# Performance work log

Measured on AMD Instinct MI355X. Metric: run time of the kernel, lower is better.

Reference implementation:

```python
import jax, jax.numpy as jnp
import numpy as np

D_MODEL = 1024
NHEAD = 16
D_K = D_MODEL // NHEAD
EPS = 1e-5


def _layernorm(x, scale, bias):
    m = jnp.mean(x, axis=-1, keepdims=True)
    v = jnp.var(x, axis=-1, keepdims=True)
    return (x - m) * jax.lax.rsqrt(v + EPS) * scale + bias


def setup_inputs() -> dict:
    key = jax.random.key(0)
    ks = jax.random.split(key, 16)
    d, h = D_MODEL, 4 * D_MODEL
    s = 1.0 / np.sqrt(d)
    inp = {
        "x": jax.random.normal(ks[0], (2, 2048, d), dtype=jnp.float32),
        "Wq": jax.random.normal(ks[1], (d, d), dtype=jnp.float32) * s,
        "bq": jnp.zeros((d,), jnp.float32),
        "Wk": jax.random.normal(ks[2], (d, d), dtype=jnp.float32) * s,
        "bk": jnp.zeros((d,), jnp.float32),
        "Wv": jax.random.normal(ks[3], (d, d), dtype=jnp.float32) * s,
        "bv": jnp.zeros((d,), jnp.float32),
        "Wo": jax.random.normal(ks[4], (d, d), dtype=jnp.float32) * s,
        "bo": jnp.zeros((d,), jnp.float32),
        "ln1_scale": jnp.ones((d,), jnp.float32),
        "ln1_bias": jnp.zeros((d,), jnp.float32),
        "ln2_scale": jnp.ones((d,), jnp.float32),
        "ln2_bias": jnp.zeros((d,), jnp.float32),
        "W1": jax.random.normal(ks[5], (d, h), dtype=jnp.float32) * s,
        "b1": jnp.zeros((h,), jnp.float32),
        "W2": jax.random.normal(ks[6], (h, d), dtype=jnp.float32) * (1.0 / np.sqrt(h)),
        "b2": jnp.zeros((d,), jnp.float32),
    }
    return inp


def reference(x, Wq, bq, Wk, bk, Wv, bv, Wo, bo,
              ln1_scale, ln1_bias, ln2_scale, ln2_bias,
              W1, b1, W2, b2):
    batch, seq, d_model = x.shape
    # Faithful to original: q is viewed WITHOUT transpose (asymmetric vs k,v)
    q = (x @ Wq + bq).reshape(batch, NHEAD, seq, D_K)
    k = (x @ Wk + bk).reshape(batch, seq, NHEAD, D_K).transpose(0, 2, 1, 3)
    v = (x @ Wv + bv).reshape(batch, seq, NHEAD, D_K).transpose(0, 2, 1, 3)
    # scores: [B, H, S, S]
    scores = jnp.einsum('bhqd,bhkd->bhqk', q, k) / np.sqrt(D_K)
    attn = jax.nn.softmax(scores, axis=-1)
    o = jnp.einsum('bhqk,bhkd->bhqd', attn, v)  # [B,H,S,dk]
    o = o.transpose(0, 2, 1, 3).reshape(batch, seq, d_model)
    x = _layernorm(x + o @ Wo + bo, ln1_scale, ln1_bias)
    ff = jax.nn.relu(x @ W1 + b1) @ W2 + b2
    x = _layernorm(x + ff, ln2_scale, ln2_bias)
    return x
```

## Files before the change

kernel.cpp:

```cpp
#include <hip/hip_runtime.h>
#include <cstdint>

typedef __bf16 bf16x8 __attribute__((ext_vector_type(8)));
typedef float  floatx4 __attribute__((ext_vector_type(4)));

__device__ __forceinline__ unsigned short f2bf(float x) {
  union { float f; uint32_t u; } v; v.f = x;
  uint32_t r = (v.u + 0x7FFFu + ((v.u >> 16) & 1u)) >> 16;
  return (unsigned short)r;
}
__device__ __forceinline__ float bflo(uint32_t u) {
  union { uint32_t u; float f; } v; v.u = u << 16; return v.f;
}
__device__ __forceinline__ float bfhi(uint32_t u) {
  union { uint32_t u; float f; } v; v.u = u & 0xffff0000u; return v.f;
}
__device__ __forceinline__ float bfu(unsigned short u) {
  union { uint32_t u; float f; } v; v.u = (uint32_t)u << 16; return v.f;
}

__device__ __forceinline__ void async_copy16(const void* g, void* l) {
  __builtin_amdgcn_global_load_lds(
      (const __attribute__((address_space(1))) uint32_t*)g,
      (__attribute__((address_space(3))) uint32_t*)l, 16, 0, 0);
}

template<int OUT_BF16, int RELU>
__global__ __launch_bounds__(256, 2)
void gemm_bt_kernel(const unsigned short* __restrict__ A,
                    const unsigned short* __restrict__ Bt,
                    void* __restrict__ C, const float* __restrict__ bias,
                    int M, int N, int K, int Kper) {
  __shared__ __align__(16) unsigned short l0A[128 * 32];
  __shared__ __align__(16) unsigned short l0B[128 * 32];
  __shared__ __align__(16) unsigned short l1A[128 * 32];
  __shared__ __align__(16) unsigned short l1B[128 * 32];
  const int tid  = threadIdx.x;
  const int wave = tid >> 6;
  const int lane = tid & 63;

  const int gx = gridDim.x, gy = gridDim.y;
  int flat = blockIdx.y * gx + blockIdx.x;
  const int per = (gx * gy) >> 3;
  flat = (flat & 7) * per + (flat >> 3);
  const int sq = flat >> 6, inner = flat & 63;
  const int sqm = gy >> 3;
  const int m0 = ((sq % sqm) * 8 + (inner & 7)) * 128;
  const int n0 = ((sq / sqm) * 8 + (inner >> 3)) * 128;

  const int kz = blockIdx.z;
  const int wm = (wave >> 1) * 64;
  const int wn = (wave & 1) * 64;
  const int sa_row = lane >> 2;
  const int sa_k   = ((lane & 3) ^ ((lane >> 3) & 3)) * 8;
  const int fr = lane & 15;
  const int fq = lane >> 4;
  const int sw = (fr >> 1) & 3;

  const int r0 = (wave * 2 + 0) * 16 + sa_row;
  const int r1 = (wave * 2 + 1) * 16 + sa_row;
  const unsigned short* A0 = A  + (size_t)(m0 + r0) * K + kz * Kper + sa_k;
  const unsigned short* A1 = A  + (size_t)(m0 + r1) * K + kz * Kper + sa_k;
  const unsigned short* B0 = Bt + (size_t)(n0 + r0) * K + kz * Kper + sa_k;
  const unsigned short* B1 = Bt + (size_t)(n0 + r1) * K + kz * Kper + sa_k;

  floatx4 acc[4][4];
  #pragma unroll
  for (int i = 0; i < 4; ++i)
    #pragma unroll
    for (int j = 0; j < 4; ++j)
      acc[i][j] = (floatx4){0.f, 0.f, 0.f, 0.f};

  const int c0 = (wave * 2 + 0) * 512;
  const int c1 = (wave * 2 + 1) * 512;

#define PREFETCH(kt, LA, LB)                                   \
  do {                                                         \
    const int koff = (kt) << 5;                                \
    async_copy16(A0 + koff, &(LA)[c0]);                        \
    async_copy16(A1 + koff, &(LA)[c1]);                        \
    async_copy16(B0 + koff, &(LB)[c0]);                        \
    async_copy16(B1 + koff, &(LB)[c1]);                        \
  } while (0)

#define COMPUTE(LA, LB)                                                        \
  do {                                                                         \
    bf16x8 af[4], bf[4];                                                       \
    _Pragma("unroll")                                                          \
    for (int t = 0; t < 4; ++t) {                                              \
      af[t] = *(const bf16x8*)&(LA)[(wm + t * 16 + fr) * 32 + (fq ^ sw) * 8];  \
      bf[t] = *(const bf16x8*)&(LB)[(wn + t * 16 + fr) * 32 + (fq ^ sw) * 8];  \
    }                                                                          \
    _Pragma("unroll")                                                          \
    for (int mt = 0; mt < 4; ++mt)                                             \
      _Pragma("unroll")                                                        \
      for (int nt = 0; nt < 4; ++nt)                                           \
        acc[mt][nt] = __builtin_amdgcn_mfma_f32_16x16x32_bf16(af[mt], bf[nt],  \
                                                              acc[mt][nt], 0, 0, 0); \
  } while (0)

  const int kIters = Kper >> 5;
  PREFETCH(0, l0A, l0B);
  for (int kt = 0; kt < kIters; kt += 2) {
    PREFETCH(kt + 1, l1A, l1B);
    asm volatile("s_waitcnt vmcnt(4)" ::: "memory");
    asm volatile("s_barrier" ::: "memory");
    COMPUTE(l0A, l0B);
    asm volatile("s_barrier" ::: "memory");
    if (kt + 2 < kIters) {
      PREFETCH(kt + 2, l0A, l0B);
      asm volatile("s_waitcnt vmcnt(4)" ::: "memory");
    } else {
      asm volatile("s_waitcnt vmcnt(0)" ::: "memory");
    }
    asm volatile("s_barrier" ::: "memory");
    COMPUTE(l1A, l1B);
    asm volatile("s_barrier" ::: "memory");
  }
#undef PREFETCH
#undef COMPUTE

  const float* bp = (kz == 0) ? bias : nullptr;
  char* Cz = (char*)C + (size_t)kz * M * N * (OUT_BF16 ? 2 : 4);
  #pragma unroll
  for (int mt = 0; mt < 4; ++mt) {
    #pragma unroll
    for (int nt = 0; nt < 4; ++nt) {
      const int gn = n0 + wn + nt * 16 + fr;
      const float bv = bp ? bp[gn] : 0.f;
      #pragma unroll
      for (int r = 0; r < 4; ++r) {
        const int gm = m0 + wm + mt * 16 + fq * 4 + r;
        float v = acc[mt][nt][r] + bv;
        if (RELU) v = fmaxf(v, 0.f);
        if (OUT_BF16) ((unsigned short*)Cz)[(size_t)gm * N + gn] = f2bf(v);
        else          ((float*)Cz)[(size_t)gm * N + gn] = v;
      }
    }
  }
}

__global__ __launch_bounds__(256, 2)
void gemm_oproj_kernel(const unsigned short* __restrict__ Opart,
                       const float* __restrict__ invL,
                       const unsigned short* __restrict__ Bt,
                       unsigned short* __restrict__ C,
                       const float* __restrict__ bias) {
  const int K = 1024, N = 1024, M = 4096, Kper = 512;
  __shared__ __align__(16) unsigned short lA[128 * 32];
  __shared__ __align__(16) unsigned short lB[128 * 32];
  const int tid  = threadIdx.x;
  const int wave = tid >> 6;
  const int lane = tid & 63;

  const int gx = gridDim.x, gy = gridDim.y;
  int flat = blockIdx.y * gx + blockIdx.x;
  const int per = (gx * gy) >> 3;
  flat = (flat & 7) * per + (flat >> 3);
  const int sq = flat >> 6, inner = flat & 63;
  const int sqm = gy >> 3;
  const int m0 = ((sq % sqm) * 8 + (inner & 7)) * 128;
  const int n0 = ((sq / sqm) * 8 + (inner >> 3)) * 128;

  const int kz = blockIdx.z;
  const int wm = (wave >> 1) * 64;
  const int wn = (wave & 1) * 64;
  const int sa_row = lane >> 2;
  const int sa_k   = ((lane & 3) ^ ((lane >> 3) & 3)) * 8;
  const int fr = lane & 15;
  const int fq = lane >> 4;
  const int sw = (fr >> 1) & 3;

  const int r0 = (wave * 2 + 0) * 16 + sa_row;
  const int r1 = (wave * 2 + 1) * 16 + sa_row;
  const int gm0 = m0 + r0, gm1 = m0 + r1;
  const int base0 = (gm0 >> 11) * 16 * 2048 + (gm0 & 2047);
  const int base1 = (gm1 >> 11) * 16 * 2048 + (gm1 & 2047);
  const unsigned short* B0 = Bt + (size_t)(n0 + r0) * K + kz * Kper + sa_k;
  const unsigned short* B1 = Bt + (size_t)(n0 + r1) * K + kz * Kper + sa_k;
  const int c0 = (wave * 2 + 0) * 512;
  const int c1 = (wave * 2 + 1) * 512;

  floatx4 acc[4][4];
  #pragma unroll
  for (int i = 0; i < 4; ++i)
    #pragma unroll
    for (int j = 0; j < 4; ++j)
      acc[i][j] = (floatx4){0.f, 0.f, 0.f, 0.f};

  for (int kt = 0; kt < 16; ++kt) {
    __syncthreads();
    const int kk = kz * Kper + (kt << 5) + sa_k;
    const int h = kk >> 6, d0 = kk & 63;
    #pragma unroll
    for (int j = 0; j < 2; ++j) {
      const int base = j ? base1 : base0;
      const int cj   = j ? c1 : c0;
      const int rowi = base + h * 2048;
      const size_t idx = (size_t)rowi * 64 + d0;
      const uint4 a = *(const uint4*)(Opart + idx);
      const uint4 b = *(const uint4*)(Opart + idx + 4194304);
      const float s = invL[rowi];
      const uint32_t au[4] = {a.x, a.y, a.z, a.w};
      const uint32_t bu[4] = {b.x, b.y, b.z, b.w};
      uint32_t w[4];
      #pragma unroll
      for (int k = 0; k < 4; ++k) {
        const float lo = (bflo(au[k]) + bflo(bu[k])) * s;
        const float hi = (bfhi(au[k]) + bfhi(bu[k])) * s;
        w[k] = (uint32_t)f2bf(lo) | ((uint32_t)f2bf(hi) << 16);
      }
      uint4 wv; wv.x = w[0]; wv.y = w[1]; wv.z = w[2]; wv.w = w[3];
      *(uint4*)&lA[cj + lane * 8] = wv;
    }
    async_copy16(B0 + (kt << 5), &lB[c0]);
    async_copy16(B1 + (kt << 5), &lB[c1]);
    __syncthreads();

    bf16x8 af[4], bf[4];
    #pragma unroll
    for (int t = 0; t < 4; ++t) {
      af[t] = *(const bf16x8*)&lA[(wm + t * 16 + fr) * 32 + (fq ^ sw) * 8];
      bf[t] = *(const bf16x8*)&lB[(wn + t * 16 + fr) * 32 + (fq ^ sw) * 8];
    }
    #pragma unroll
    for (int mt = 0; mt < 4; ++mt)
      #pragma unroll
      for (int nt = 0; nt < 4; ++nt)
        acc[mt][nt] = __builtin_amdgcn_mfma_f32_16x16x32_bf16(af[mt], bf[nt], acc[mt][nt], 0, 0, 0);
  }

  const float* bp = (kz == 0) ? bias : nullptr;
  unsigned short* Cz = C + (size_t)kz * M * N;
  #pragma unroll
  for (int mt = 0; mt < 4; ++mt) {
    #pragma unroll
    for (int nt = 0; nt < 4; ++nt) {
      const int gn = n0 + wn + nt * 16 + fr;
      const float bv = bp ? bp[gn] : 0.f;
      #pragma unroll
      for (int r = 0; r < 4; ++r) {
        const int gm = m0 + wm + mt * 16 + fq * 4 + r;
        Cz[(size_t)gm * N + gn] = f2bf(acc[mt][nt][r] + bv);
      }
    }
  }
}

__global__ __launch_bounds__(256)
void repack_v_kernel(const unsigned short* __restrict__ X,
                     unsigned short* __restrict__ Vt) {
  const int bid = blockIdx.x;
  const int st = bid & 31, h = (bid >> 5) & 15, b = bid >> 9;
  const int bh = b * 16 + h;
  const int s0 = st * 64;
  const int t = threadIdx.x;
  const int sl = t >> 2;
  const int c  = (t & 3) * 16;
  __shared__ __align__(16) unsigned short vt[64][72];
  {
    const uint4* srcV = (const uint4*)(X + (size_t)(b * 2048 + s0 + sl) * 3072 + 2048 + h * 64 + c);
    uint4* dstL = (uint4*)&vt[sl][c];
    dstL[0] = srcV[0]; dstL[1] = srcV[1];
  }
  __syncthreads();
  const int d = t >> 2, cc = (t & 3) * 16;
  unsigned short tmp[16];
  #pragma unroll
  for (int j = 0; j < 16; ++j) {
    const int chat = cc + j;
    const int key = (chat & 3) * 16 + (chat >> 2);
    tmp[j] = vt[key][d];
  }
  uint4* dstV = (uint4*)(Vt + ((size_t)bh * 64 + d) * 2048 + s0 + cc);
  dstV[0] = *(uint4*)&tmp[0];
  dstV[1] = *(uint4*)&tmp[8];
}

__global__ __launch_bounds__(256, 4)
void flash_attn_kernel(const unsigned short* __restrict__ QKVb,
                       const unsigned short* __restrict__ Vt,
                       unsigned short* __restrict__ Opart, float* __restrict__ Lpart) {
  const int bid = blockIdx.x;
  const int qt = bid & 15, h = (bid >> 4) & 15, b = (bid >> 8) & 1, ksp = bid >> 9;
  const int bh = b * 16 + h;
  const int wave = threadIdx.x >> 6, lane = threadIdx.x & 63;
  const int fr = lane & 15, fq = lane >> 4;

  __shared__ __align__(16) unsigned short lK[64 * 64];
  __shared__ __align__(16) unsigned short lV[64 * 64];
  __shared__ __align__(16) unsigned short lP[4][32 * 72];

  const int q_base = qt * 128 + wave * 32;
  bf16x8 aq[2][2];
  #pragma unroll
  for (int g = 0; g < 2; ++g) {
    const int s2 = q_base + g * 16 + fr;
    const unsigned short* qp = QKVb + (size_t)(b * 2048 + h * 128 + (s2 >> 4)) * 3072
                             + (s2 & 15) * 64 + fq * 8;
    aq[g][0] = *(const bf16x8*)qp;
    aq[g][1] = *(const bf16x8*)(qp + 32);
  }
  floatx4 o_acc[2][4];
  #pragma unroll
  for (int g = 0; g < 2; ++g)
    #pragma unroll
    for (int nt = 0; nt < 4; ++nt) o_acc[g][nt] = (floatx4){0.f, 0.f, 0.f, 0.f};
  float lrow[2][4];
  #pragma unroll
  for (int g = 0; g < 2; ++g)
    #pragma unroll
    for (int r = 0; r < 4; ++r) lrow[g][r] = 0.f;

  const unsigned short* Kg = QKVb + 1024 + h * 64;
  const unsigned short* Vg = Vt + (size_t)bh * 64 * 2048;

  const int srow = lane >> 3;
  const int scol = ((lane & 7) ^ (lane >> 3)) * 8;
  const int sw = fr & 7;
  const int ch0 = wave * 2, ch1 = wave * 2 + 1;
  const int krow0 = ch0 * 8 + srow, krow1 = ch1 * 8 + srow;

  for (int kt = ksp * 16; kt < ksp * 16 + 16; ++kt) {
    __syncthreads();
    async_copy16(Kg + (size_t)(b * 2048 + kt * 64 + krow0) * 3072 + scol, (char*)lK + ch0 * 1024);
    async_copy16(Vg + (size_t)krow0 * 2048 + kt * 64 + scol,              (char*)lV + ch0 * 1024);
    async_copy16(Kg + (size_t)(b * 2048 + kt * 64 + krow1) * 3072 + scol, (char*)lK + ch1 * 1024);
    async_copy16(Vg + (size_t)krow1 * 2048 + kt * 64 + scol,              (char*)lV + ch1 * 1024);
    asm volatile("s_waitcnt vmcnt(0)" ::: "memory");
    __syncthreads();

    floatx4 s_acc[2][4];
    #pragma unroll
    for (int nt = 0; nt < 4; ++nt) {
      const int row = (nt * 16 + fr) * 64;
      bf16x8 bk0 = *(const bf16x8*)&lK[row + ((0 + fq) ^ sw) * 8];
      bf16x8 bk1 = *(const bf16x8*)&lK[row + ((4 + fq) ^ sw) * 8];
      #pragma unroll
      for (int g = 0; g < 2; ++g) {
        floatx4 acc = (floatx4){0.f, 0.f, 0.f, 0.f};
        acc = __builtin_amdgcn_mfma_f32_16x16x32_bf16(aq[g][0], bk0, acc, 0, 0, 0);
        acc = __builtin_amdgcn_mfma_f32_16x16x32_bf16(aq[g][1], bk1, acc, 0, 0, 0);
        s_acc[g][nt] = acc;
      }
    }
    bf16x8 bvv[2][4];
    #pragma unroll
    for (int kk = 0; kk < 2; ++kk)
      #pragma unroll
      for (int nt = 0; nt < 4; ++nt)
        bvv[kk][nt] = *(const bf16x8*)&lV[(nt * 16 + fr) * 64 + ((kk * 4 + fq) ^ sw) * 8];

    #pragma unroll
    for (int g = 0; g < 2; ++g) {
      #pragma unroll
      for (int r = 0; r < 4; ++r) {
        const float p0 = __builtin_amdgcn_exp2f(s_acc[g][0][r] * 0.18033688f);
        const float p1 = __builtin_amdgcn_exp2f(s_acc[g][1][r] * 0.18033688f);
        const float p2 = __builtin_amdgcn_exp2f(s_acc[g][2][r] * 0.18033688f);
        const float p3 = __builtin_amdgcn_exp2f(s_acc[g][3][r] * 0.18033688f);
        lrow[g][r] += (p0 + p1) + (p2 + p3);
        union { float f; uint32_t u; } c0, c1, c2, c3;
        c0.f = p0; c1.f = p1; c2.f = p2; c3.f = p3;
        uint2 pk;
        pk.x = (c1.u & 0xffff0000u) | (c0.u >> 16);
        pk.y = (c3.u & 0xffff0000u) | (c2.u >> 16);
        *(uint2*)&lP[wave][(g * 16 + fq * 4 + r) * 72 + fr * 4] = pk;
      }
    }
    #pragma unroll
    for (int g = 0; g < 2; ++g) {
      #pragma unroll
      for (int kk = 0; kk < 2; ++kk) {
        bf16x8 ap = *(const bf16x8*)&lP[wave][(g * 16 + fr) * 72 + kk * 32 + fq * 8];
        #pragma unroll
        for (int nt = 0; nt < 4; ++nt)
          o_acc[g][nt] = __builtin_amdgcn_mfma_f32_16x16x32_bf16(ap, bvv[kk][nt], o_acc[g][nt], 0, 0, 0);
      }
    }
  }

  const size_t rbase = (size_t)ksp * 65536 + (size_t)bh * 2048 + q_base;
  #pragma unroll
  for (int g = 0; g < 2; ++g) {
    #pragma unroll
    for (int r = 0; r < 4; ++r) {
      float l = lrow[g][r];
      #pragma unroll
      for (int off = 1; off < 16; off <<= 1) l += __shfl_xor(l, off);
      if (fr == 0) Lpart[rbase + g * 16 + fq * 4 + r] = l;
    }
    #pragma unroll
    for (int nt = 0; nt < 4; ++nt)
      #pragma unroll
      for (int r = 0; r < 4; ++r)
        Opart[(rbase + g * 16 + fq * 4 + r) * 64 + nt * 16 + fr] = f2bf(o_acc[g][nt][r]);
  }
}

__global__ __launch_bounds__(256)
void invl_kernel(const float* __restrict__ Lpart, float* __restrict__ invL) {
  const int i = blockIdx.x * 256 + threadIdx.x;
  invL[i] = 1.f / (Lpart[i] + Lpart[i + 65536]);
}

template<int XF32, int OUTF32>
__global__ __launch_bounds__(256)
void ln_kernel(const void* __restrict__ Xv, const unsigned short* __restrict__ R,
               const unsigned short* __restrict__ R2,
               const float* __restrict__ sc, const float* __restrict__ bi,
               float* __restrict__ outF, unsigned short* __restrict__ outB) {
  const int row = blockIdx.x;
  const int t = threadIdx.x;
  const size_t base = (size_t)row * 1024 + t * 4;
  float4 a;
  if (XF32) {
    a = *(const float4*)((const float*)Xv + base);
  } else {
    const ushort4 xu = *(const ushort4*)((const unsigned short*)Xv + base);
    a.x = bfu(xu.x); a.y = bfu(xu.y); a.z = bfu(xu.z); a.w = bfu(xu.w);
  }
  const ushort4 r1u = *(const ushort4*)&R[base];
  const ushort4 r2u = *(const ushort4*)&R2[base];
  a.x += bfu(r1u.x) + bfu(r2u.x);
  a.y += bfu(r1u.y) + bfu(r2u.y);
  a.z += bfu(r1u.z) + bfu(r2u.z);
  a.w += bfu(r1u.w) + bfu(r2u.w);
  float sum = (a.x + a.y) + (a.z + a.w);
  float sq  = (a.x * a.x + a.y * a.y) + (a.z * a.z + a.w * a.w);
  #pragma unroll
  for (int off = 32; off > 0; off >>= 1) {
    sum += __shfl_down(sum, off);
    sq  += __shfl_down(sq, off);
  }
  __shared__ float s1[4], s2a[4];
  const int wave = t >> 6, lane = t & 63;
  if (lane == 0) { s1[wave] = sum; s2a[wave] = sq; }
  __syncthreads();
  sum = (s1[0] + s1[1]) + (s1[2] + s1[3]);
  sq  = (s2a[0] + s2a[1]) + (s2a[2] + s2a[3]);
  const float mean = sum * (1.f / 1024.f);
  const float var  = sq * (1.f / 1024.f) - mean * mean;
  const float rstd = rsqrtf(var + 1e-5f);
  const float4 s = *(const float4*)&sc[t * 4];
  const float4 bb = *(const float4*)&bi[t * 4];
  float4 y;
  y.x = (a.x - mean) * rstd * s.x + bb.x;
  y.y = (a.y - mean) * rstd * s.y + bb.y;
  y.z = (a.z - mean) * rstd * s.z + bb.z;
  y.w = (a.w - mean) * rstd * s.w + bb.w;
  if (OUTF32) {
    *(float4*)&outF[base] = y;
  } else {
    ushort4 ob; ob.x = f2bf(y.x); ob.y = f2bf(y.y); ob.z = f2bf(y.z); ob.w = f2bf(y.w);
    *(ushort4*)&outB[base] = ob;
  }
}

__global__ void prep_kernel(const float* __restrict__ Wq, const float* __restrict__ Wk,
                            const float* __restrict__ Wv, const float* __restrict__ Wo,
                            const float* __restrict__ W1, const float* __restrict__ W2,
                            unsigned short* __restrict__ Wqkvt, unsigned short* __restrict__ Wot,
                            unsigned short* __restrict__ W1t, unsigned short* __restrict__ W2t,
                            const float* __restrict__ x, unsigned short* __restrict__ xb,
                            const float* __restrict__ bq, const float* __restrict__ bk,
                            const float* __restrict__ bv, float* __restrict__ bqkv) {
  const int id = blockIdx.x;
  const int tflat = threadIdx.y * 32 + threadIdx.x;
  if (id >= 16384) {
    const int i = (id - 16384) * 256 + tflat;
    if (i < 1024) bqkv[i] = bq[i];
    else if (i < 2048) bqkv[i] = bk[i - 1024];
    else if (i < 3072) bqkv[i] = bv[i - 2048];
    return;
  }
  if (id >= 12288) {
    const int i = (id - 12288) * 256 + tflat;
    const float4 v = ((const float4*)x)[i];
    ushort4 o;
    o.x = f2bf(v.x); o.y = f2bf(v.y); o.z = f2bf(v.z); o.w = f2bf(v.w);
    ((ushort4*)xb)[i] = o;
    return;
  }
  const float* W; unsigned short* Wt; int K, N, tile;
  if (id < 4096) {
    const int w = id >> 10; tile = id & 1023; K = 1024; N = 1024;
    if (w == 0)      { W = Wq; Wt = Wqkvt; }
    else if (w == 1) { W = Wk; Wt = Wqkvt + 1024 * 1024; }
    else if (w == 2) { W = Wv; Wt = Wqkvt + 2048 * 1024; }
    else             { W = Wo; Wt = Wot; }
  } else if (id < 8192) { tile = id - 4096; W = W1; Wt = W1t; K = 1024; N = 4096; }
  else                  { tile = id - 8192; W = W2; Wt = W2t; K = 4096; N = 1024; }
  const int tilesX = N >> 5;
  const int bx = (tile & (tilesX - 1)) * 32;
  const int by = (tile / tilesX) * 32;
  __shared__ float tl[32][33];
  const int tx = threadIdx.x, ty = threadIdx.y;
  #pragma unroll
  for (int i = ty; i < 32; i += 8)
    tl[i][tx] = W[(size_t)(by + i) * N + bx + tx];
  __syncthreads();
  #pragma unroll
  for (int i = ty; i < 32; i += 8)
    Wt[(size_t)(bx + i) * K + by + tx] = f2bf(tl[tx][i]);
}

extern "C" void kernel_launch(void* const* d_in, const int* in_sizes, int n_in,
                              void* d_out, int out_size, void* d_ws, size_t ws_size,
                              hipStream_t stream) {
  const float* x    = (const float*)d_in[0];
  const float* Wq   = (const float*)d_in[1];
  const float* bq   = (const float*)d_in[2];
  const float* Wk   = (const float*)d_in[3];
  const float* bk   = (const float*)d_in[4];
  const float* Wv   = (const float*)d_in[5];
  const float* bv   = (const float*)d_in[6];
  const float* Wo   = (const float*)d_in[7];
  const float* bo   = (const float*)d_in[8];
  const float* ln1s = (const float*)d_in[9];
  const float* ln1b = (const float*)d_in[10];
  const float* ln2s = (const float*)d_in[11];
  const float* ln2b = (const float*)d_in[12];
  const float* W1   = (const float*)d_in[13];
  const float* b1   = (const float*)d_in[14];
  const float* W2   = (const float*)d_in[15];
  const float* b2   = (const float*)d_in[16];
  float* out = (float*)d_out;

  char* ws = (char*)d_ws;
  const size_t MB = 1u << 20;
  unsigned short* QKVb = (unsigned short*)(ws + 0);
  unsigned short* t1   = (unsigned short*)(ws + 0);
  unsigned short* ffh  = (unsigned short*)(ws + 0);
  unsigned short* Vt   = (unsigned short*)(ws + 32 * MB);
  unsigned short* ff   = (unsigned short*)(ws + 32 * MB);
  unsigned short* xb   = (unsigned short*)(ws + 48 * MB);
  unsigned short* Opart= (unsigned short*)(ws + 48 * MB);
  unsigned short* Wqkvt= (unsigned short*)(ws + 56 * MB);
  float*          Lpart= (float*)(ws + 80 * MB);
  float*          invL = (float*)(ws + 80 * MB + 512 * 1024);
  unsigned short* Wot  = (unsigned short*)(ws + 81 * MB);
  unsigned short* W1t  = (unsigned short*)(ws + 83 * MB);
  unsigned short* W2t  = (unsigned short*)(ws + 91 * MB);
  float*          bqkv = (float*)(ws + 99 * MB);
  unsigned short* x1b  = (unsigned short*)(ws + 100 * MB);

  prep_kernel<<<16396, dim3(32, 8), 0, stream>>>(Wq, Wk, Wv, Wo, W1, W2,
                                                 Wqkvt, Wot, W1t, W2t,
                                                 x, xb, bq, bk, bv, bqkv);
  gemm_bt_kernel<1, 0><<<dim3(24, 32, 1), 256, 0, stream>>>(xb, Wqkvt, QKVb, bqkv, 4096, 3072, 1024, 1024);
  repack_v_kernel<<<1024, 256, 0, stream>>>(QKVb, Vt);
  flash_attn_kernel<<<1024, 256, 0, stream>>>(QKVb, Vt, Opart, Lpart);
  invl_kernel<<<256, 256, 0, stream>>>(Lpart, invL);
  gemm_oproj_kernel<<<dim3(8, 32, 2), 256, 0, stream>>>(Opart, invL, Wot, t1, bo);
  ln_kernel<1, 0><<<4096, 256, 0, stream>>>(x, t1, t1 + 4096 * 1024, ln1s, ln1b, nullptr, x1b);
  gemm_bt_kernel<1, 1><<<dim3(32, 32, 1), 256, 0, stream>>>(x1b, W1t, ffh, b1, 4096, 4096, 1024, 1024);
  gemm_bt_kernel<1, 0><<<dim3(8, 32, 2), 256, 0, stream>>>(ffh, W2t, ff, b2, 4096, 1024, 4096, 2048);
  ln_kernel<0, 1><<<4096, 256, 0, stream>>>(x1b, ff, ff + 4096 * 1024, ln2s, ln2b, out, nullptr);

  (void)in_sizes; (void)n_in; (void)out_size; (void)ws_size;
}
```

Baseline: 362.4 us.

## Double-buffer flash attention K/V, fold softmax scale into Wq, widen split-K

```diff
diff --git a/kernel.cpp b/kernel.cpp
--- a/kernel.cpp
+++ b/kernel.cpp
@@ -18,6 +18,8 @@
 __device__ __forceinline__ float bfu(unsigned short u) {
   union { uint32_t u; float f; } v; v.u = (uint32_t)u << 16; return v.f;
 }
+
+#define QSCALE 0.18033688011f
 
 __device__ __forceinline__ void async_copy16(const void* g, void* l) {
   __builtin_amdgcn_global_load_lds(
@@ -146,7 +148,7 @@
                        const unsigned short* __restrict__ Bt,
                        unsigned short* __restrict__ C,
                        const float* __restrict__ bias) {
-  const int K = 1024, N = 1024, M = 4096, Kper = 512;
+  const int K = 1024, N = 1024, M = 4096, Kper = 256;
   __shared__ __align__(16) unsigned short lA[128 * 32];
   __shared__ __align__(16) unsigned short lB[128 * 32];
   const int tid  = threadIdx.x;
@@ -188,7 +190,7 @@
     for (int j = 0; j < 4; ++j)
       acc[i][j] = (floatx4){0.f, 0.f, 0.f, 0.f};
 
-  for (int kt = 0; kt < 16; ++kt) {
+  for (int kt = 0; kt < 8; ++kt) {
     __syncthreads();
     const int kk = kz * Kper + (kt << 5) + sa_k;
     const int h = kk >> 6, d0 = kk & 63;
@@ -268,8 +270,9 @@
   unsigned short tmp[16];
   #pragma unroll
   for (int j = 0; j < 16; ++j) {
-    const int chat = cc + j;
-    const int key = (chat & 3) * 16 + (chat >> 2);
+    const int c64 = cc + j;
+    const int grp = c64 >> 5, cw = c64 & 31;
+    const int key = grp * 32 + (cw & 1) * 16 + (cw >> 1);
     tmp[j] = vt[key][d];
   }
   uint4* dstV = (uint4*)(Vt + ((size_t)bh * 64 + d) * 2048 + s0 + cc);
@@ -287,9 +290,9 @@
   const int wave = threadIdx.x >> 6, lane = threadIdx.x & 63;
   const int fr = lane & 15, fq = lane >> 4;
 
-  __shared__ __align__(16) unsigned short lK[64 * 64];
-  __shared__ __align__(16) unsigned short lV[64 * 64];
-  __shared__ __align__(16) unsigned short lP[4][32 * 72];
+  __shared__ __align__(16) unsigned short lK[2][32 * 64];
+  __shared__ __align__(16) unsigned short lV[2][64 * 32];
+  __shared__ __align__(16) unsigned short lP[4][32 * 40];
 
   const int q_base = qt * 128 + wave * 32;
   bf16x8 aq[2][2];
@@ -315,69 +318,84 @@
   const unsigned short* Kg = QKVb + 1024 + h * 64;
   const unsigned short* Vg = Vt + (size_t)bh * 64 * 2048;
 
-  const int srow = lane >> 3;
-  const int scol = ((lane & 7) ^ (lane >> 3)) * 8;
-  const int sw = fr & 7;
-  const int ch0 = wave * 2, ch1 = wave * 2 + 1;
-  const int krow0 = ch0 * 8 + srow, krow1 = ch1 * 8 + srow;
-
-  for (int kt = ksp * 16; kt < ksp * 16 + 16; ++kt) {
-    __syncthreads();
-    async_copy16(Kg + (size_t)(b * 2048 + kt * 64 + krow0) * 3072 + scol, (char*)lK + ch0 * 1024);
-    async_copy16(Vg + (size_t)krow0 * 2048 + kt * 64 + scol,              (char*)lV + ch0 * 1024);
-    async_copy16(Kg + (size_t)(b * 2048 + kt * 64 + krow1) * 3072 + scol, (char*)lK + ch1 * 1024);
-    async_copy16(Vg + (size_t)krow1 * 2048 + kt * 64 + scol,              (char*)lV + ch1 * 1024);
-    asm volatile("s_waitcnt vmcnt(0)" ::: "memory");
-    __syncthreads();
-
-    floatx4 s_acc[2][4];
-    #pragma unroll
-    for (int nt = 0; nt < 4; ++nt) {
+  const int krow = wave * 8 + (lane >> 3);
+  const int kcol = ((lane & 7) ^ (lane >> 3)) * 8;
+  const unsigned short* Ksrc = Kg + (size_t)(b * 2048 + krow) * 3072 + kcol;
+  const int vd   = wave * 16 + (lane >> 2);
+  const int vcol = ((lane & 3) ^ ((lane >> 3) & 3)) * 8;
+  const unsigned short* Vsrc = Vg + (size_t)vd * 2048 + vcol;
+
+  auto pref = [&](int key0, int bi) {
+    async_copy16(Ksrc + (size_t)key0 * 3072, (char*)lK[bi] + wave * 1024);
+    async_copy16(Vsrc + key0,                (char*)lV[bi] + wave * 1024);
+  };
+
+  const int swk = fr & 7;
+  const int swv = (fr >> 1) & 3;
+
+  auto compute_half = [&](const unsigned short* LK, const unsigned short* LV) {
+    bf16x8 bk0[2], bk1[2];
+    #pragma unroll
+    for (int nt = 0; nt < 2; ++nt) {
       const int row = (nt * 16 + fr) * 64;
-      bf16x8 bk0 = *(const bf16x8*)&lK[row + ((0 + fq) ^ sw) * 8];
-      bf16x8 bk1 = *(const bf16x8*)&lK[row + ((4 + fq) ^ sw) * 8];
+      bk0[nt] = *(const bf16x8*)&LK[row + ((0 + fq) ^ swk) * 8];
+      bk1[nt] = *(const bf16x8*)&LK[row + ((4 + fq) ^ swk) * 8];
+    }
+    floatx4 s_acc[2][2];
+    #pragma unroll
+    for (int nt = 0; nt < 2; ++nt)
       #pragma unroll
       for (int g = 0; g < 2; ++g) {
         floatx4 acc = (floatx4){0.f, 0.f, 0.f, 0.f};
-        acc = __builtin_amdgcn_mfma_f32_16x16x32_bf16(aq[g][0], bk0, acc, 0, 0, 0);
-        acc = __builtin_amdgcn_mfma_f32_16x16x32_bf16(aq[g][1], bk1, acc, 0, 0, 0);
+        acc = __builtin_amdgcn_mfma_f32_16x16x32_bf16(aq[g][0], bk0[nt], acc, 0, 0, 0);
+        acc = __builtin_amdgcn_mfma_f32_16x16x32_bf16(aq[g][1], bk1[nt], acc, 0, 0, 0);
         s_acc[g][nt] = acc;
       }
-    }
-    bf16x8 bvv[2][4];
-    #pragma unroll
-    for (int kk = 0; kk < 2; ++kk)
+    bf16x8 bv[4];
+    #pragma unroll
+    for (int nt = 0; nt < 4; ++nt) {
+      const int d = nt * 16 + fr;
+      bv[nt] = *(const bf16x8*)&LV[d * 32 + (fq ^ swv) * 8];
+    }
+    #pragma unroll
+    for (int g = 0; g < 2; ++g) {
+      #pragma unroll
+      for (int r = 0; r < 4; ++r) {
+        const float p0 = __builtin_amdgcn_exp2f(s_acc[g][0][r]);
+        const float p1 = __builtin_amdgcn_exp2f(s_acc[g][1][r]);
+        lrow[g][r] += p0 + p1;
+        union { float f; uint32_t u; } z0, z1;
+        z0.f = p0; z1.f = p1;
+        *(uint32_t*)&lP[wave][(g * 16 + fq * 4 + r) * 40 + fr * 2] =
+            (z1.u & 0xffff0000u) | (z0.u >> 16);
+      }
+    }
+    #pragma unroll
+    for (int g = 0; g < 2; ++g) {
+      bf16x8 ap = *(const bf16x8*)&lP[wave][(g * 16 + fr) * 40 + fq * 8];
       #pragma unroll
       for (int nt = 0; nt < 4; ++nt)
-        bvv[kk][nt] = *(const bf16x8*)&lV[(nt * 16 + fr) * 64 + ((kk * 4 + fq) ^ sw) * 8];
-
-    #pragma unroll
-    for (int g = 0; g < 2; ++g) {
-      #pragma unroll
-      for (int r = 0; r < 4; ++r) {
-        const float p0 = __builtin_amdgcn_exp2f(s_acc[g][0][r] * 0.18033688f);
-        const float p1 = __builtin_amdgcn_exp2f(s_acc[g][1][r] * 0.18033688f);
-        const float p2 = __builtin_amdgcn_exp2f(s_acc[g][2][r] * 0.18033688f);
-        const float p3 = __builtin_amdgcn_exp2f(s_acc[g][3][r] * 0.18033688f);
-        lrow[g][r] += (p0 + p1) + (p2 + p3);
-        union { float f; uint32_t u; } c0, c1, c2, c3;
-        c0.f = p0; c1.f = p1; c2.f = p2; c3.f = p3;
-        uint2 pk;
-        pk.x = (c1.u & 0xffff0000u) | (c0.u >> 16);
-        pk.y = (c3.u & 0xffff0000u) | (c2.u >> 16);
-        *(uint2*)&lP[wave][(g * 16 + fq * 4 + r) * 72 + fr * 4] = pk;
-      }
-    }
-    #pragma unroll
-    for (int g = 0; g < 2; ++g) {
-      #pragma unroll
-      for (int kk = 0; kk < 2; ++kk) {
-        bf16x8 ap = *(const bf16x8*)&lP[wave][(g * 16 + fr) * 72 + kk * 32 + fq * 8];
-        #pragma unroll
-        for (int nt = 0; nt < 4; ++nt)
-          o_acc[g][nt] = __builtin_amdgcn_mfma_f32_16x16x32_bf16(ap, bvv[kk][nt], o_acc[g][nt], 0, 0, 0);
-      }
-    }
+        o_acc[g][nt] = __builtin_amdgcn_mfma_f32_16x16x32_bf16(ap, bv[nt], o_acc[g][nt], 0, 0, 0);
+    }
+  };
+
+  const int key00 = ksp * 1024;
+  pref(key00, 0);
+  for (int hh = 0; hh < 32; hh += 2) {
+    pref(key00 + (hh + 1) * 32, 1);
+    asm volatile("s_waitcnt vmcnt(2)" ::: "memory");
+    asm volatile("s_barrier" ::: "memory");
+    compute_half(lK[0], lV[0]);
+    asm volatile("s_barrier" ::: "memory");
+    if (hh + 2 < 32) {
+      pref(key00 + (hh + 2) * 32, 0);
+      asm volatile("s_waitcnt vmcnt(2)" ::: "memory");
+    } else {
+      asm volatile("s_waitcnt vmcnt(0)" ::: "memory");
+    }
+    asm volatile("s_barrier" ::: "memory");
+    compute_half(lK[1], lV[1]);
+    asm volatile("s_barrier" ::: "memory");
   }
 
   const size_t rbase = (size_t)ksp * 65536 + (size_t)bh * 2048 + q_base;
@@ -404,10 +422,9 @@
   invL[i] = 1.f / (Lpart[i] + Lpart[i + 65536]);
 }
 
-template<int XF32, int OUTF32>
+template<int XF32, int OUTF32, int NPART>
 __global__ __launch_bounds__(256)
 void ln_kernel(const void* __restrict__ Xv, const unsigned short* __restrict__ R,
-               const unsigned short* __restrict__ R2,
                const float* __restrict__ sc, const float* __restrict__ bi,
                float* __restrict__ outF, unsigned short* __restrict__ outB) {
   const int row = blockIdx.x;
@@ -420,12 +437,11 @@
     const ushort4 xu = *(const ushort4*)((const unsigned short*)Xv + base);
     a.x = bfu(xu.x); a.y = bfu(xu.y); a.z = bfu(xu.z); a.w = bfu(xu.w);
   }
-  const ushort4 r1u = *(const ushort4*)&R[base];
-  const ushort4 r2u = *(const ushort4*)&R2[base];
-  a.x += bfu(r1u.x) + bfu(r2u.x);
-  a.y += bfu(r1u.y) + bfu(r2u.y);
-  a.z += bfu(r1u.z) + bfu(r2u.z);
-  a.w += bfu(r1u.w) + bfu(r2u.w);
+  #pragma unroll
+  for (int p = 0; p < NPART; ++p) {
+    const ushort4 ru = *(const ushort4*)&R[(size_t)p * 4194304 + base];
+    a.x += bfu(ru.x); a.y += bfu(ru.y); a.z += bfu(ru.z); a.w += bfu(ru.w);
+  }
   float sum = (a.x + a.y) + (a.z + a.w);
   float sq  = (a.x * a.x + a.y * a.y) + (a.z * a.z + a.w * a.w);
   #pragma unroll
@@ -469,7 +485,7 @@
   const int tflat = threadIdx.y * 32 + threadIdx.x;
   if (id >= 16384) {
     const int i = (id - 16384) * 256 + tflat;
-    if (i < 1024) bqkv[i] = bq[i];
+    if (i < 1024) bqkv[i] = bq[i] * QSCALE;
     else if (i < 2048) bqkv[i] = bk[i - 1024];
     else if (i < 3072) bqkv[i] = bv[i - 2048];
     return;
@@ -483,9 +499,10 @@
     return;
   }
   const float* W; unsigned short* Wt; int K, N, tile;
+  float scale = 1.f;
   if (id < 4096) {
     const int w = id >> 10; tile = id & 1023; K = 1024; N = 1024;
-    if (w == 0)      { W = Wq; Wt = Wqkvt; }
+    if (w == 0)      { W = Wq; Wt = Wqkvt; scale = QSCALE; }
     else if (w == 1) { W = Wk; Wt = Wqkvt + 1024 * 1024; }
     else if (w == 2) { W = Wv; Wt = Wqkvt + 2048 * 1024; }
     else             { W = Wo; Wt = Wot; }
@@ -502,7 +519,7 @@
   __syncthreads();
   #pragma unroll
   for (int i = ty; i < 32; i += 8)
-    Wt[(size_t)(bx + i) * K + by + tx] = f2bf(tl[tx][i]);
+    Wt[(size_t)(bx + i) * K + by + tx] = f2bf(tl[tx][i] * scale);
 }
 
 extern "C" void kernel_launch(void* const* d_in, const int* in_sizes, int n_in,
@@ -552,11 +569,11 @@
   repack_v_kernel<<<1024, 256, 0, stream>>>(QKVb, Vt);
   flash_attn_kernel<<<1024, 256, 0, stream>>>(QKVb, Vt, Opart, Lpart);
   invl_kernel<<<256, 256, 0, stream>>>(Lpart, invL);
-  gemm_oproj_kernel<<<dim3(8, 32, 2), 256, 0, stream>>>(Opart, invL, Wot, t1, bo);
-  ln_kernel<1, 0><<<4096, 256, 0, stream>>>(x, t1, t1 + 4096 * 1024, ln1s, ln1b, nullptr, x1b);
+  gemm_oproj_kernel<<<dim3(8, 32, 4), 256, 0, stream>>>(Opart, invL, Wot, t1, bo);
+  ln_kernel<1, 0, 4><<<4096, 256, 0, stream>>>(x, t1, ln1s, ln1b, nullptr, x1b);
   gemm_bt_kernel<1, 1><<<dim3(32, 32, 1), 256, 0, stream>>>(x1b, W1t, ffh, b1, 4096, 4096, 1024, 1024);
-  gemm_bt_kernel<1, 0><<<dim3(8, 32, 2), 256, 0, stream>>>(ffh, W2t, ff, b2, 4096, 1024, 4096, 2048);
-  ln_kernel<0, 1><<<4096, 256, 0, stream>>>(x1b, ff, ff + 4096 * 1024, ln2s, ln2b, out, nullptr);
+  gemm_bt_kernel<1, 0><<<dim3(8, 32, 4), 256, 0, stream>>>(ffh, W2t, ff, b2, 4096, 1024, 4096, 1024);
+  ln_kernel<0, 1, 4><<<4096, 256, 0, stream>>>(x1b, ff, ln2s, ln2b, out, nullptr);
 
   (void)in_sizes; (void)n_in; (void)out_size; (void)ws_size;
 }
```

Result: no change. 358.5 us (-1.1%).
